# Performance work log

Measured on AMD Instinct MI355X. Metric: run time of the kernel, lower is better.

Reference implementation:

```python
import jax, jax.numpy as jnp
import numpy as np

K = 7      # kernel_size (local window)
PAD = 3    # (K - 1) // 2 so output spatial == input spatial
CIN = 256
COUT = 256
B, H, W = 2, 48, 48


def _unfold2d(x, k):
    """x: [B, C, Hp, Wp] -> sliding windows [B, C, H, W, kh, kw] (stride 1)."""
    Hout = x.shape[2] - k + 1
    Wout = x.shape[3] - k + 1
    rows = jnp.stack([x[:, :, i:i + Hout, :] for i in range(k)], axis=-1)   # [B,C,H,Wp,kh]
    return jnp.stack([rows[:, :, :, j:j + Wout, :] for j in range(k)], axis=-1)  # [B,C,H,W,kh,kw]


def setup_inputs() -> dict:
    key = jax.random.key(0)
    ks = jax.random.split(key, 6)
    s = 1.0 / np.sqrt(CIN)
    return {
        "x": jax.random.normal(ks[0], (B, CIN, H, W), jnp.float32),
        "w_q": jax.random.normal(ks[1], (COUT, CIN), jnp.float32) * s,
        "w_k": jax.random.normal(ks[2], (COUT, CIN), jnp.float32) * s,
        "w_v": jax.random.normal(ks[3], (COUT, CIN), jnp.float32) * s,
        "rel_h": jax.random.normal(ks[4], (COUT // 2, 1, 1, K, 1), jnp.float32),
        "rel_w": jax.random.normal(ks[5], (COUT // 2, 1, 1, 1, K), jnp.float32),
    }


def reference(x, w_q, w_k, w_v, rel_h, rel_w):
    b, cin, h, w = x.shape
    cout = w_q.shape[0]
    half = cout // 2
    # 1x1 convs == channel GEMMs
    x_pad = jnp.pad(x, ((0, 0), (0, 0), (PAD, PAD), (PAD, PAD)))
    q = jnp.einsum('bchw,oc->bohw', x, w_q)          # [B,Cout,H,W]
    kmap = jnp.einsum('bchw,oc->bohw', x_pad, w_k)   # [B,Cout,H+2p,W+2p]
    vmap = jnp.einsum('bchw,oc->bohw', x_pad, w_v)
    # local windows (torch .unfold(2,k,1).unfold(3,k,1))
    kwin = _unfold2d(kmap, K)   # [B,Cout,H,W,kh,kw]
    vwin = _unfold2d(vmap, K)
    # relative position bias: first half channels biased over kh, second over kw
    kwin = jnp.concatenate([kwin[:, :half] + rel_h, kwin[:, half:] + rel_w], axis=1)
    kwin = kwin.reshape(b, cout, h, w, K * K)
    vwin = vwin.reshape(b, cout, h, w, K * K)
    # per-channel, per-position attention over the k*k window
    attn = jax.nn.softmax(q[..., None] * kwin, axis=-1)
    out = jnp.sum(attn * vwin, axis=-1)              # [B,Cout,H,W]
    return out
```

## Files before the change

### kernel.cpp

```cpp
#include <hip/hip_runtime.h>

#define CIN  256
#define COUT 256
#define BSZ  2
#define HH   48
#define WW   48
#define S    (HH * WW)
#define KWIN 7

typedef short  short8 __attribute__((ext_vector_type(8)));
typedef float  f32x4  __attribute__((ext_vector_type(4)));

__device__ inline unsigned cvt_pk_bf16(float f0, float f1) {
    unsigned r;
    asm("v_cvt_pk_bf16_f32 %0, %1, %2" : "=v"(r) : "v"(f0), "v"(f1));
    return r;
}

__global__ __launch_bounds__(256) void qkv_mfma(
    const float* __restrict__ x,
    const float* __restrict__ wq, const float* __restrict__ wk, const float* __restrict__ wv,
    float* __restrict__ qout, float* __restrict__ kout, float* __restrict__ vout)
{
    __shared__ __align__(16) short Ahi[32][64][8];
    __shared__ __align__(16) short Alo[32][64][8];
    const int t    = threadIdx.x;
    const int lane = t & 63;
    const int wid  = t >> 6;
    const int r16  = lane & 15;
    const int kq   = lane >> 4;
    const int s0   = blockIdx.x * 64;
    const int o0   = blockIdx.y * 128 + wid * 32;
    const int bm   = blockIdx.z;
    const int b    = bm / 3, m = bm % 3;
    const float* wmat = (m == 0) ? wq : (m == 1 ? wk : wv);
    float* outp = ((m == 0) ? qout : (m == 1 ? kout : vout)) + (size_t)b * COUT * S;
    const float* xb = x + (size_t)b * CIN * S + s0;

    const int ss = t & 63;
    const int cg = t >> 6;
#pragma unroll 2
    for (int p = 0; p < 8; ++p) {
        const int c8 = cg + p * 4;
        const float* px = xb + (size_t)(c8 * 8) * S + ss;
        float f[8];
#pragma unroll
        for (int e = 0; e < 8; ++e) f[e] = px[(size_t)e * S];
        union { unsigned u[4]; short8 v; } H, L;
#pragma unroll
        for (int pp = 0; pp < 4; ++pp) {
            H.u[pp] = cvt_pk_bf16(f[2 * pp], f[2 * pp + 1]);
            const float h0 = __uint_as_float(H.u[pp] << 16);
            const float h1 = __uint_as_float(H.u[pp] & 0xFFFF0000u);
            L.u[pp] = cvt_pk_bf16(f[2 * pp] - h0, f[2 * pp + 1] - h1);
        }
        *(short8*)&Ahi[c8][ss][0] = H.v;
        *(short8*)&Alo[c8][ss][0] = L.v;
    }
    __syncthreads();

    f32x4 acc[4][2] = {};
#pragma unroll 2
    for (int kb = 0; kb < 8; ++kb) {
        const int c8 = kb * 4 + kq;
        short8 ah[4], al[4], bh[2];
#pragma unroll
        for (int i = 0; i < 4; ++i) {
            ah[i] = *(const short8*)&Ahi[c8][i * 16 + r16][0];
            al[i] = *(const short8*)&Alo[c8][i * 16 + r16][0];
        }
#pragma unroll
        for (int j = 0; j < 2; ++j) {
            const float* pw = wmat + (size_t)(o0 + j * 16 + r16) * CIN + kb * 32 + kq * 8;
            const float4 wa = *(const float4*)pw;
            const float4 wb = *(const float4*)(pw + 4);
            union { unsigned u[4]; short8 v; } B;
            B.u[0] = cvt_pk_bf16(wa.x, wa.y);
            B.u[1] = cvt_pk_bf16(wa.z, wa.w);
            B.u[2] = cvt_pk_bf16(wb.x, wb.y);
            B.u[3] = cvt_pk_bf16(wb.z, wb.w);
            bh[j] = B.v;
        }
#pragma unroll
        for (int i = 0; i < 4; ++i)
#pragma unroll
            for (int j = 0; j < 2; ++j) {
                acc[i][j] = __builtin_amdgcn_mfma_f32_16x16x32_bf16(ah[i], bh[j], acc[i][j], 0, 0, 0);
                acc[i][j] = __builtin_amdgcn_mfma_f32_16x16x32_bf16(al[i], bh[j], acc[i][j], 0, 0, 0);
            }
    }
#pragma unroll
    for (int i = 0; i < 4; ++i)
#pragma unroll
        for (int j = 0; j < 2; ++j) {
            const int o = o0 + j * 16 + r16;
            const int s = s0 + i * 16 + kq * 4;
            float4 r = make_float4(acc[i][j][0], acc[i][j][1], acc[i][j][2], acc[i][j][3]);
            *(float4*)(outp + (size_t)o * S + s) = r;
        }
}

__global__ __launch_bounds__(192) void attn_win(
    const float* __restrict__ qmap,
    const float* __restrict__ kmap,
    const float* __restrict__ vmap,
    const float* __restrict__ rel_h,
    const float* __restrict__ rel_w,
    float* __restrict__ out)
{
    __shared__ __align__(16) float Ks[14][60];
    __shared__ __align__(16) float Vs[14][60];
    const int t  = threadIdx.x;
    const int h0 = blockIdx.x * 8;
    const int bo = blockIdx.y;
    const int o  = bo & 255;
    const float* kp = kmap + (size_t)bo * S;
    const float* vp = vmap + (size_t)bo * S;

    for (int i = t; i < 14 * 56; i += 192) {
        const int row = i / 56, col = i - row * 56;
        const int hh = h0 - 3 + row, ww = col - 3;
        const bool ok = ((unsigned)hh < (unsigned)HH) && ((unsigned)ww < (unsigned)WW);
        Ks[row][col] = ok ? kp[hh * WW + ww] : 0.f;
        Vs[row][col] = ok ? vp[hh * WW + ww] : 0.f;
    }

    const int w0 = (t % 24) * 2;
    const int r  = t / 24;
    const int h  = h0 + r;
    const float2 q2 = *(const float2*)(qmap + (size_t)bo * S + h * WW + w0);
    const float qe0 = q2.x * 1.44269504088896340736f;
    const float qe1 = q2.y * 1.44269504088896340736f;
    const bool ish = (o < 128);
    const float* rp = ish ? (rel_h + o * 7) : (rel_w + (o - 128) * 7);
    float rel[7];
#pragma unroll
    for (int i = 0; i < 7; ++i) rel[i] = rp[i];

    __syncthreads();

    float l0 = 0.f, l1 = 0.f, a0 = 0.f, a1 = 0.f;
#pragma unroll
    for (int kh = 0; kh < KWIN; ++kh) {
        const int rr = r + kh;
        float k8[8], v8[8];
#pragma unroll
        for (int n = 0; n < 4; ++n) {
            *(float2*)&k8[2 * n] = *(const float2*)&Ks[rr][w0 + 2 * n];
            *(float2*)&v8[2 * n] = *(const float2*)&Vs[rr][w0 + 2 * n];
        }
        if (ish) {
            const float b0 = qe0 * rel[kh];
            const float b1 = qe1 * rel[kh];
#pragma unroll
            for (int kw = 0; kw < KWIN; ++kw) {
                const float p0 = __builtin_amdgcn_exp2f(fmaf(qe0, k8[kw], b0));
                l0 += p0; a0 = fmaf(p0, v8[kw], a0);
                const float p1 = __builtin_amdgcn_exp2f(fmaf(qe1, k8[kw + 1], b1));
                l1 += p1; a1 = fmaf(p1, v8[kw + 1], a1);
            }
        } else {
#pragma unroll
            for (int kw = 0; kw < KWIN; ++kw) {
                const float p0 = __builtin_amdgcn_exp2f(fmaf(qe0, k8[kw], qe0 * rel[kw]));
                l0 += p0; a0 = fmaf(p0, v8[kw], a0);
                const float p1 = __builtin_amdgcn_exp2f(fmaf(qe1, k8[kw + 1], qe1 * rel[kw]));
                l1 += p1; a1 = fmaf(p1, v8[kw + 1], a1);
            }
        }
    }
    float r0, r1;
    asm("v_rcp_f32 %0, %1" : "=v"(r0) : "v"(l0));
    asm("v_rcp_f32 %0, %1" : "=v"(r1) : "v"(l1));
    float2 ov = make_float2(a0 * r0, a1 * r1);
    *(float2*)(out + (size_t)bo * S + h * WW + w0) = ov;
}

extern "C" void kernel_launch(void* const* d_in, const int* in_sizes, int n_in,
                              void* d_out, int out_size, void* d_ws, size_t ws_size,
                              hipStream_t stream) {
    const float* x     = (const float*)d_in[0];
    const float* wq    = (const float*)d_in[1];
    const float* wk    = (const float*)d_in[2];
    const float* wv    = (const float*)d_in[3];
    const float* rel_h = (const float*)d_in[4];
    const float* rel_w = (const float*)d_in[5];
    float* out  = (float*)d_out;

    float* kbuf = (float*)d_ws;
    float* vbuf = kbuf + (size_t)BSZ * COUT * S;

    dim3 gg(S / 64, COUT / 128, BSZ * 3);
    qkv_mfma<<<gg, 256, 0, stream>>>(x, wq, wk, wv, out, kbuf, vbuf);

    dim3 g2(HH / 8, BSZ * COUT);
    attn_win<<<g2, 192, 0, stream>>>(out, kbuf, vbuf, rel_h, rel_w, out);
}
```

Baseline: 37.69 us.

## Halve QKV GEMM spatial tile and vectorize attention halo loads

```diff
diff --git a/kernel.cpp b/kernel.cpp
--- a/kernel.cpp
+++ b/kernel.cpp
@@ -22,14 +22,14 @@
     const float* __restrict__ wq, const float* __restrict__ wk, const float* __restrict__ wv,
     float* __restrict__ qout, float* __restrict__ kout, float* __restrict__ vout)
 {
-    __shared__ __align__(16) short Ahi[32][64][8];
-    __shared__ __align__(16) short Alo[32][64][8];
+    __shared__ __align__(16) short Ahi[32][32][8];
+    __shared__ __align__(16) short Alo[32][32][8];
     const int t    = threadIdx.x;
     const int lane = t & 63;
     const int wid  = t >> 6;
     const int r16  = lane & 15;
     const int kq   = lane >> 4;
-    const int s0   = blockIdx.x * 64;
+    const int s0   = blockIdx.x * 32;
     const int o0   = blockIdx.y * 128 + wid * 32;
     const int bm   = blockIdx.z;
     const int b    = bm / 3, m = bm % 3;
@@ -37,11 +37,11 @@
     float* outp = ((m == 0) ? qout : (m == 1 ? kout : vout)) + (size_t)b * COUT * S;
     const float* xb = x + (size_t)b * CIN * S + s0;
 
-    const int ss = t & 63;
-    const int cg = t >> 6;
+    const int ss = t & 31;
+    const int cg = t >> 5;
 #pragma unroll 2
-    for (int p = 0; p < 8; ++p) {
-        const int c8 = cg + p * 4;
+    for (int p = 0; p < 4; ++p) {
+        const int c8 = cg * 4 + p;
         const float* px = xb + (size_t)(c8 * 8) * S + ss;
         float f[8];
 #pragma unroll
@@ -59,13 +59,13 @@
     }
     __syncthreads();
 
-    f32x4 acc[4][2] = {};
+    f32x4 acc[2][2] = {};
 #pragma unroll 2
     for (int kb = 0; kb < 8; ++kb) {
         const int c8 = kb * 4 + kq;
-        short8 ah[4], al[4], bh[2];
-#pragma unroll
-        for (int i = 0; i < 4; ++i) {
+        short8 ah[2], al[2], bh[2];
+#pragma unroll
+        for (int i = 0; i < 2; ++i) {
             ah[i] = *(const short8*)&Ahi[c8][i * 16 + r16][0];
             al[i] = *(const short8*)&Alo[c8][i * 16 + r16][0];
         }
@@ -82,7 +82,7 @@
             bh[j] = B.v;
         }
 #pragma unroll
-        for (int i = 0; i < 4; ++i)
+        for (int i = 0; i < 2; ++i)
 #pragma unroll
             for (int j = 0; j < 2; ++j) {
                 acc[i][j] = __builtin_amdgcn_mfma_f32_16x16x32_bf16(ah[i], bh[j], acc[i][j], 0, 0, 0);
@@ -90,7 +90,7 @@
             }
     }
 #pragma unroll
-    for (int i = 0; i < 4; ++i)
+    for (int i = 0; i < 2; ++i)
 #pragma unroll
         for (int j = 0; j < 2; ++j) {
             const int o = o0 + j * 16 + r16;
@@ -117,12 +117,18 @@
     const float* kp = kmap + (size_t)bo * S;
     const float* vp = vmap + (size_t)bo * S;
 
-    for (int i = t; i < 14 * 56; i += 192) {
-        const int row = i / 56, col = i - row * 56;
-        const int hh = h0 - 3 + row, ww = col - 3;
-        const bool ok = ((unsigned)hh < (unsigned)HH) && ((unsigned)ww < (unsigned)WW);
-        Ks[row][col] = ok ? kp[hh * WW + ww] : 0.f;
-        Vs[row][col] = ok ? vp[hh * WW + ww] : 0.f;
+    const float4 z4 = make_float4(0.f, 0.f, 0.f, 0.f);
+    for (int i = t; i < 420; i += 192) {
+        const int a   = (i >= 210);
+        const int j   = i - 210 * a;
+        const int row = j / 15;
+        const int c4  = j - row * 15;
+        const int hh  = h0 - 3 + row;
+        const bool ok = (c4 >= 1) && (c4 <= 12) && ((unsigned)hh < (unsigned)HH);
+        const float* src = a ? vp : kp;
+        const float4 val = ok ? *(const float4*)(src + hh * WW + (c4 - 1) * 4) : z4;
+        float* dst = a ? &Vs[row][c4 * 4] : &Ks[row][c4 * 4];
+        *(float4*)dst = val;
     }
 
     const int w0 = (t % 24) * 2;
@@ -133,9 +139,13 @@
     const float qe1 = q2.y * 1.44269504088896340736f;
     const bool ish = (o < 128);
     const float* rp = ish ? (rel_h + o * 7) : (rel_w + (o - 128) * 7);
-    float rel[7];
-#pragma unroll
-    for (int i = 0; i < 7; ++i) rel[i] = rp[i];
+    float rel[7], qr0[7], qr1[7];
+#pragma unroll
+    for (int i = 0; i < 7; ++i) {
+        rel[i] = rp[i];
+        qr0[i] = qe0 * rel[i];
+        qr1[i] = qe1 * rel[i];
+    }
 
     __syncthreads();
 
@@ -145,13 +155,13 @@
         const int rr = r + kh;
         float k8[8], v8[8];
 #pragma unroll
-        for (int n = 0; n < 4; ++n) {
-            *(float2*)&k8[2 * n] = *(const float2*)&Ks[rr][w0 + 2 * n];
-            *(float2*)&v8[2 * n] = *(const float2*)&Vs[rr][w0 + 2 * n];
+        for (int n = 0; n < 8; ++n) {
+            k8[n] = Ks[rr][w0 + 1 + n];
+            v8[n] = Vs[rr][w0 + 1 + n];
         }
         if (ish) {
-            const float b0 = qe0 * rel[kh];
-            const float b1 = qe1 * rel[kh];
+            const float b0 = qr0[kh];
+            const float b1 = qr1[kh];
 #pragma unroll
             for (int kw = 0; kw < KWIN; ++kw) {
                 const float p0 = __builtin_amdgcn_exp2f(fmaf(qe0, k8[kw], b0));
@@ -162,9 +172,9 @@
         } else {
 #pragma unroll
             for (int kw = 0; kw < KWIN; ++kw) {
-                const float p0 = __builtin_amdgcn_exp2f(fmaf(qe0, k8[kw], qe0 * rel[kw]));
+                const float p0 = __builtin_amdgcn_exp2f(fmaf(qe0, k8[kw], qr0[kw]));
                 l0 += p0; a0 = fmaf(p0, v8[kw], a0);
-                const float p1 = __builtin_amdgcn_exp2f(fmaf(qe1, k8[kw + 1], qe1 * rel[kw]));
+                const float p1 = __builtin_amdgcn_exp2f(fmaf(qe1, k8[kw + 1], qr1[kw]));
                 l1 += p1; a1 = fmaf(p1, v8[kw + 1], a1);
             }
         }
@@ -190,7 +200,7 @@
     float* kbuf = (float*)d_ws;
     float* vbuf = kbuf + (size_t)BSZ * COUT * S;
 
-    dim3 gg(S / 64, COUT / 128, BSZ * 3);
+    dim3 gg(S / 32, COUT / 128, BSZ * 3);
     qkv_mfma<<<gg, 256, 0, stream>>>(x, wq, wk, wv, out, kbuf, vbuf);
 
     dim3 g2(HH / 8, BSZ * COUT);
```

After: 54.85 us. +45.5%, slower.
